# Kernel tuning notes

Hardware: AMD Instinct MI355X
Metric: run time of the kernel (lower is better)

The kernel has to match this reference:

```python
import jax, jax.numpy as jnp
import numpy as np

B, T, C = 2048, 200, 128
PAD = jnp.float32(-4294967295.0)  # -(2**32) + 1, as in SoftmaxWeightedSum padding


def setup_inputs() -> dict:
    key = jax.random.key(0)
    k1, k2, k3, k4 = jax.random.split(key, 4)
    user_query = jax.random.normal(k1, (B, 1, C), dtype=jnp.float32)
    keys = jax.random.normal(k2, (B, T, C), dtype=jnp.float32)
    keys_length = jax.random.randint(k3, (B, 1), 0, T, dtype=jnp.int32)
    W = jax.random.normal(k4, (C, C), dtype=jnp.float32) * (1.0 / np.sqrt(C))
    b = jnp.zeros((C,), dtype=jnp.float32)
    return {"user_query": user_query, "keys": keys, "keys_length": keys_length, "W": W, "b": b}


def reference(user_query, keys, keys_length, W, b):
    # Dense with tanh activation: [B,1,C] -> [B,1,C]
    query = jnp.tanh(jnp.einsum('bqc,cd->bqd', user_query, W) + b)
    # DotAttention with scale: [B,1,T]
    scale = jnp.asarray(1.0 / np.sqrt(C), dtype=keys.dtype)
    align = jnp.einsum('bqc,btc->bqt', query, keys) * scale
    # sequence mask [B,1,T] from keys_length [B,1]
    key_masks = jnp.arange(T, dtype=keys_length.dtype)[None, None, :] < keys_length[:, :, None]
    align = jnp.where(key_masks, align, PAD)
    align = jax.nn.softmax(align, axis=-1)
    # weighted sum over history: [B,1,C]
    output = jnp.einsum('bqt,btc->bqc', align, keys)
    # residual: broadcasts [B,1,C] + [B,T,C] -> [B,T,C] (faithful to `output += keys`)
    output = output + keys
    # mean pool over sequence, keepdims -> [B,1,C]
    return jnp.mean(output, axis=1, keepdims=True)
```

## Files before the change

### kernel.cpp

```cpp
#include <hip/hip_runtime.h>
#include <math.h>

#define BB 2048
#define TT 200
#define CC 128
#define PADV (-4294967295.0f)
#define SCALE 0.08838834764831845f
#define INVT (1.0f / 200.0f)

__global__ __launch_bounds__(256) void user_attn_kernel(
    const float* __restrict__ uq,
    const float* __restrict__ keys,
    const int*   __restrict__ klen,
    const float* __restrict__ W,
    const float* __restrict__ bias,
    float*       __restrict__ out)
{
    const int b    = blockIdx.x;
    const int tid  = threadIdx.x;
    const int lane = tid & 63;
    const int wid  = tid >> 6;

    __shared__ float  s_q[CC];
    __shared__ float  s_w[TT];
    __shared__ float  s_uq[CC];
    __shared__ float  s_tmp[8];
    __shared__ float2 s_acc[256];

    const float* kb = keys + (size_t)b * TT * CC;

    if (tid < CC) s_uq[tid] = uq[b * CC + tid];
    __syncthreads();
    if (tid < CC) {
        float acc = bias[tid];
        #pragma unroll 8
        for (int c = 0; c < CC; ++c)
            acc = fmaf(s_uq[c], W[c * CC + tid], acc);
        s_q[tid] = tanhf(acc);
    }
    __syncthreads();

    const int len = klen[b];

    const float q0 = s_q[2 * lane];
    const float q1 = s_q[2 * lane + 1];
    for (int t = wid; t < TT; t += 4) {
        const float2 k = *(const float2*)(kb + t * CC + 2 * lane);
        float d = q0 * k.x + q1 * k.y;
        #pragma unroll
        for (int off = 32; off > 0; off >>= 1)
            d += __shfl_xor(d, off, 64);
        if (lane == 0)
            s_w[t] = (t < len) ? d * SCALE : PADV;
    }
    __syncthreads();

    float v = (tid < TT) ? s_w[tid] : -INFINITY;
    float m = v;
    #pragma unroll
    for (int off = 32; off > 0; off >>= 1)
        m = fmaxf(m, __shfl_xor(m, off, 64));
    if (lane == 0) s_tmp[wid] = m;
    __syncthreads();
    m = fmaxf(fmaxf(s_tmp[0], s_tmp[1]), fmaxf(s_tmp[2], s_tmp[3]));

    float e = (tid < TT) ? expf(v - m) : 0.0f;
    float ssum = e;
    #pragma unroll
    for (int off = 32; off > 0; off >>= 1)
        ssum += __shfl_xor(ssum, off, 64);
    if (lane == 0) s_tmp[4 + wid] = ssum;
    __syncthreads();
    ssum = s_tmp[4] + s_tmp[5] + s_tmp[6] + s_tmp[7];
    if (tid < TT) s_w[tid] = e / ssum + INVT;
    __syncthreads();

    const int c2 = lane * 2;
    float2 acc = make_float2(0.0f, 0.0f);
    for (int t = wid; t < TT; t += 4) {
        const float w  = s_w[t];
        const float2 k = *(const float2*)(kb + t * CC + c2);
        acc.x = fmaf(w, k.x, acc.x);
        acc.y = fmaf(w, k.y, acc.y);
    }
    s_acc[tid] = acc;
    __syncthreads();
    if (tid < 64) {
        float2 r  = s_acc[tid];
        float2 a1 = s_acc[tid + 64];
        float2 a2 = s_acc[tid + 128];
        float2 a3 = s_acc[tid + 192];
        r.x += a1.x + a2.x + a3.x;
        r.y += a1.y + a2.y + a3.y;
        *(float2*)(out + (size_t)b * CC + c2) = r;
    }
}

extern "C" void kernel_launch(void* const* d_in, const int* in_sizes, int n_in,
                              void* d_out, int out_size, void* d_ws, size_t ws_size,
                              hipStream_t stream) {
    const float* uq   = (const float*)d_in[0];
    const float* keys = (const float*)d_in[1];
    const int*   klen = (const int*)d_in[2];
    const float* W    = (const float*)d_in[3];
    const float* bias = (const float*)d_in[4];
    float* out = (float*)d_out;

    user_attn_kernel<<<BB, 256, 0, stream>>>(uq, keys, klen, W, bias, out);
}
```

Baseline: 329.2 us.

## Cache keys in shared memory as bf16 to avoid second global read

Each key row is now read from global memory once. The kernel converts the keys to bf16 and stages them in LDS, and the weighted-sum pass reads that copy instead of re-fetching them from HBM. The block grows to 512 threads, the W·q matvec is split across four thread groups, and loads widen to float4. Rounding the keys to bf16 lowers the precision of the weighted sum, and the roughly 53KB of LDS per block may cut occupancy.

```diff
diff --git a/kernel.cpp b/kernel.cpp
--- a/kernel.cpp
+++ b/kernel.cpp
@@ -1,4 +1,5 @@
 #include <hip/hip_runtime.h>
+#include <hip/hip_bf16.h>
 #include <math.h>
 
 #define BB 2048
@@ -7,8 +8,9 @@
 #define PADV (-4294967295.0f)
 #define SCALE 0.08838834764831845f
 #define INVT (1.0f / 200.0f)
+#define PITCH 132
 
-__global__ __launch_bounds__(256) void user_attn_kernel(
+__global__ __launch_bounds__(512) void user_attn_kernel(
     const float* __restrict__ uq,
     const float* __restrict__ keys,
     const int*   __restrict__ klen,
@@ -21,78 +23,119 @@
     const int lane = tid & 63;
     const int wid  = tid >> 6;
 
-    __shared__ float  s_q[CC];
-    __shared__ float  s_w[TT];
-    __shared__ float  s_uq[CC];
-    __shared__ float  s_tmp[8];
-    __shared__ float2 s_acc[256];
+    __shared__ unsigned short s_kb16[TT * PITCH];
+    __shared__ float s_q[CC];
+    __shared__ float s_w[TT];
+    __shared__ float s_tmp[16];
+
+    float*  s_part = (float*)s_kb16;
+    float*  s_uq   = (float*)s_kb16 + 512;
+    float4* s_red  = (float4*)s_kb16;
 
     const float* kb = keys + (size_t)b * TT * CC;
 
     if (tid < CC) s_uq[tid] = uq[b * CC + tid];
     __syncthreads();
+    {
+        const int d    = tid & 127;
+        const int part = tid >> 7;
+        float acc = 0.0f;
+        const int c0 = part * 32;
+        #pragma unroll 8
+        for (int c = 0; c < 32; ++c)
+            acc = fmaf(s_uq[c0 + c], W[(c0 + c) * CC + d], acc);
+        s_part[part * CC + d] = acc;
+    }
+    __syncthreads();
     if (tid < CC) {
-        float acc = bias[tid];
-        #pragma unroll 8
-        for (int c = 0; c < CC; ++c)
-            acc = fmaf(s_uq[c], W[c * CC + tid], acc);
+        float acc = bias[tid] + s_part[tid] + s_part[CC + tid]
+                  + s_part[2 * CC + tid] + s_part[3 * CC + tid];
         s_q[tid] = tanhf(acc);
     }
     __syncthreads();
 
     const int len = klen[b];
 
-    const float q0 = s_q[2 * lane];
-    const float q1 = s_q[2 * lane + 1];
-    for (int t = wid; t < TT; t += 4) {
-        const float2 k = *(const float2*)(kb + t * CC + 2 * lane);
-        float d = q0 * k.x + q1 * k.y;
+    const int cl = lane & 31;
+    const int c4 = cl * 4;
+    const int h  = lane >> 5;
+    const float q0 = s_q[c4], q1 = s_q[c4 + 1], q2 = s_q[c4 + 2], q3 = s_q[c4 + 3];
+
+    for (int p = wid; p < TT / 2; p += 8) {
+        const int r = 2 * p + h;
+        const float4 k = *(const float4*)(kb + r * CC + c4);
+        float d = q0 * k.x + q1 * k.y + q2 * k.z + q3 * k.w;
         #pragma unroll
-        for (int off = 32; off > 0; off >>= 1)
+        for (int off = 1; off < 32; off <<= 1)
             d += __shfl_xor(d, off, 64);
-        if (lane == 0)
-            s_w[t] = (t < len) ? d * SCALE : PADV;
+        if (cl == 0)
+            s_w[r] = (r < len) ? d * SCALE : PADV;
+
+        __hip_bfloat16 h0 = __float2bfloat16(k.x);
+        __hip_bfloat16 h1 = __float2bfloat16(k.y);
+        __hip_bfloat16 h2 = __float2bfloat16(k.z);
+        __hip_bfloat16 h3 = __float2bfloat16(k.w);
+        ushort4 pk;
+        pk.x = *(unsigned short*)&h0; pk.y = *(unsigned short*)&h1;
+        pk.z = *(unsigned short*)&h2; pk.w = *(unsigned short*)&h3;
+        *(ushort4*)(&s_kb16[(size_t)r * PITCH + c4]) = pk;
     }
     __syncthreads();
 
-    float v = (tid < TT) ? s_w[tid] : -INFINITY;
-    float m = v;
-    #pragma unroll
-    for (int off = 32; off > 0; off >>= 1)
-        m = fmaxf(m, __shfl_xor(m, off, 64));
-    if (lane == 0) s_tmp[wid] = m;
-    __syncthreads();
-    m = fmaxf(fmaxf(s_tmp[0], s_tmp[1]), fmaxf(s_tmp[2], s_tmp[3]));
+    {
+        float v = (tid < TT) ? s_w[tid] : -INFINITY;
+        float m = v;
+        #pragma unroll
+        for (int off = 1; off < 64; off <<= 1)
+            m = fmaxf(m, __shfl_xor(m, off, 64));
+        if (lane == 0) s_tmp[wid] = m;
+        __syncthreads();
+        m = s_tmp[0];
+        #pragma unroll
+        for (int w = 1; w < 8; ++w) m = fmaxf(m, s_tmp[w]);
 
-    float e = (tid < TT) ? expf(v - m) : 0.0f;
-    float ssum = e;
-    #pragma unroll
-    for (int off = 32; off > 0; off >>= 1)
-        ssum += __shfl_xor(ssum, off, 64);
-    if (lane == 0) s_tmp[4 + wid] = ssum;
-    __syncthreads();
-    ssum = s_tmp[4] + s_tmp[5] + s_tmp[6] + s_tmp[7];
-    if (tid < TT) s_w[tid] = e / ssum + INVT;
+        float e = (tid < TT) ? expf(v - m) : 0.0f;
+        float ssum = e;
+        #pragma unroll
+        for (int off = 1; off < 64; off <<= 1)
+            ssum += __shfl_xor(ssum, off, 64);
+        if (lane == 0) s_tmp[8 + wid] = ssum;
+        __syncthreads();
+        ssum = 0.0f;
+        #pragma unroll
+        for (int w = 0; w < 8; ++w) ssum += s_tmp[8 + w];
+        if (tid < TT) s_w[tid] = e / ssum + INVT;
+    }
     __syncthreads();
 
-    const int c2 = lane * 2;
-    float2 acc = make_float2(0.0f, 0.0f);
-    for (int t = wid; t < TT; t += 4) {
-        const float w  = s_w[t];
-        const float2 k = *(const float2*)(kb + t * CC + c2);
-        acc.x = fmaf(w, k.x, acc.x);
-        acc.y = fmaf(w, k.y, acc.y);
+    float4 acc = make_float4(0.0f, 0.0f, 0.0f, 0.0f);
+    for (int p = wid; p < TT / 2; p += 8) {
+        const int r = 2 * p + h;
+        const float w = s_w[r];
+        const ushort4 pk = *(const ushort4*)(&s_kb16[(size_t)r * PITCH + c4]);
+        acc.x = fmaf(w, __uint_as_float((unsigned)pk.x << 16), acc.x);
+        acc.y = fmaf(w, __uint_as_float((unsigned)pk.y << 16), acc.y);
+        acc.z = fmaf(w, __uint_as_float((unsigned)pk.z << 16), acc.z);
+        acc.w = fmaf(w, __uint_as_float((unsigned)pk.w << 16), acc.w);
     }
-    s_acc[tid] = acc;
+    acc.x += __shfl_xor(acc.x, 32, 64);
+    acc.y += __shfl_xor(acc.y, 32, 64);
+    acc.z += __shfl_xor(acc.z, 32, 64);
+    acc.w += __shfl_xor(acc.w, 32, 64);
+
     __syncthreads();
-    if (tid < 64) {
-        float2 r  = s_acc[tid];
-        float2 a1 = s_acc[tid + 64];
-        float2 a2 = s_acc[tid + 128];
-        float2 a3 = s_acc[tid + 192];
-        r.x += a1.x + a2.x + a3.x;
-        r.y += a1.y + a2.y + a3.y;
-        *(float2*)(out + (size_t)b * CC + c2) = r;
+    if (cl == lane)
+        s_red[wid * 32 + cl] = acc;
+    __syncthreads();
+
+    if (tid < 32) {
+        float4 r = s_red[tid];
+        #pragma unroll
+        for (int w = 1; w < 8; ++w) {
+            float4 v = s_red[w * 32 + tid];
+            r.x += v.x; r.y += v.y; r.z += v.z; r.w += v.w;
+        }
+        *(float4*)(out + (size_t)b * CC + 4 * tid) = r;
     }
 }
 
@@ -106,5 +149,5 @@
     const float* bias = (const float*)d_in[4];
     float* out = (float*)d_out;
 
-    user_attn_kernel<<<BB, 256, 0, stream>>>(uq, keys, klen, W, bias, out);
+    user_attn_kernel<<<BB, 512, 0, stream>>>(uq, keys, klen, W, bias, out);
 }
```

Result: faster. 306.2 us (-7.0%).

## Use float4 key loads with half-wave rows and split query GEMV across all threads

Applied to the files above, without the earlier changes.

Keys are now read as float4, so each half-wave of 32 lanes covers one 128-wide row and a wavefront handles two rows per load. The score pass is unrolled to two row pairs per iteration to keep more loads in flight. The query matvec is split across all 256 threads into two partial sums that are combined before the tanh. Launch bounds now request 8 blocks per SM, and the final reduction uses float4 plus a cross-half shuffle, at the cost of shuffle reductions with more steps and possible register pressure.

```diff
diff --git a/kernel.cpp b/kernel.cpp
--- a/kernel.cpp
+++ b/kernel.cpp
@@ -8,7 +8,7 @@
 #define SCALE 0.08838834764831845f
 #define INVT (1.0f / 200.0f)
 
-__global__ __launch_bounds__(256) void user_attn_kernel(
+__global__ __launch_bounds__(256, 8) void user_attn_kernel(
     const float* __restrict__ uq,
     const float* __restrict__ keys,
     const int*   __restrict__ klen,
@@ -20,79 +20,122 @@
     const int tid  = threadIdx.x;
     const int lane = tid & 63;
     const int wid  = tid >> 6;
+    const int cl   = lane & 31;
+    const int h    = lane >> 5;
+    const int c4   = cl * 4;
 
     __shared__ float  s_q[CC];
+    __shared__ float  s_uq[CC];
+    __shared__ float  s_part[2 * CC];
     __shared__ float  s_w[TT];
-    __shared__ float  s_uq[CC];
     __shared__ float  s_tmp[8];
-    __shared__ float2 s_acc[256];
+    __shared__ float4 s_red[4 * 32];
 
     const float* kb = keys + (size_t)b * TT * CC;
 
     if (tid < CC) s_uq[tid] = uq[b * CC + tid];
     __syncthreads();
-    if (tid < CC) {
-        float acc = bias[tid];
-        #pragma unroll 8
-        for (int c = 0; c < CC; ++c)
-            acc = fmaf(s_uq[c], W[c * CC + tid], acc);
-        s_q[tid] = tanhf(acc);
+    {
+        const int d    = tid & 127;
+        const int part = tid >> 7;
+        const int c0   = part * 64;
+        float acc = 0.0f;
+        #pragma unroll 16
+        for (int c = 0; c < 64; ++c)
+            acc = fmaf(s_uq[c0 + c], W[(c0 + c) * CC + d], acc);
+        s_part[part * CC + d] = acc;
+    }
+    __syncthreads();
+    if (tid < CC)
+        s_q[tid] = tanhf(bias[tid] + s_part[tid] + s_part[CC + tid]);
+    __syncthreads();
+
+    const int len = klen[b];
+    const float q0 = s_q[c4], q1 = s_q[c4 + 1], q2 = s_q[c4 + 2], q3 = s_q[c4 + 3];
+
+    {
+        int p = wid;
+        for (; p + 4 < TT / 2; p += 8) {
+            const int r0 = 2 * p + h;
+            const int r1 = r0 + 8;
+            const float4 k0 = *(const float4*)(kb + r0 * CC + c4);
+            const float4 k1 = *(const float4*)(kb + r1 * CC + c4);
+            float d0 = q0 * k0.x + q1 * k0.y + q2 * k0.z + q3 * k0.w;
+            float d1 = q0 * k1.x + q1 * k1.y + q2 * k1.z + q3 * k1.w;
+            #pragma unroll
+            for (int off = 1; off < 32; off <<= 1) {
+                d0 += __shfl_xor(d0, off, 64);
+                d1 += __shfl_xor(d1, off, 64);
+            }
+            if (cl == 0) {
+                s_w[r0] = (r0 < len) ? d0 * SCALE : PADV;
+                s_w[r1] = (r1 < len) ? d1 * SCALE : PADV;
+            }
+        }
+        if (p < TT / 2) {
+            const int r0 = 2 * p + h;
+            const float4 k0 = *(const float4*)(kb + r0 * CC + c4);
+            float d0 = q0 * k0.x + q1 * k0.y + q2 * k0.z + q3 * k0.w;
+            #pragma unroll
+            for (int off = 1; off < 32; off <<= 1)
+                d0 += __shfl_xor(d0, off, 64);
+            if (cl == 0)
+                s_w[r0] = (r0 < len) ? d0 * SCALE : PADV;
+        }
     }
     __syncthreads();
 
-    const int len = klen[b];
+    {
+        float v = (tid < TT) ? s_w[tid] : -INFINITY;
+        float m = v;
+        #pragma unroll
+        for (int off = 1; off < 64; off <<= 1)
+            m = fmaxf(m, __shfl_xor(m, off, 64));
+        if (lane == 0) s_tmp[wid] = m;
+        __syncthreads();
+        m = fmaxf(fmaxf(s_tmp[0], s_tmp[1]), fmaxf(s_tmp[2], s_tmp[3]));
 
-    const float q0 = s_q[2 * lane];
-    const float q1 = s_q[2 * lane + 1];
-    for (int t = wid; t < TT; t += 4) {
-        const float2 k = *(const float2*)(kb + t * CC + 2 * lane);
-        float d = q0 * k.x + q1 * k.y;
+        float e = (tid < TT) ? expf(v - m) : 0.0f;
+        float ssum = e;
         #pragma unroll
-        for (int off = 32; off > 0; off >>= 1)
-            d += __shfl_xor(d, off, 64);
-        if (lane == 0)
-            s_w[t] = (t < len) ? d * SCALE : PADV;
+        for (int off = 1; off < 64; off <<= 1)
+            ssum += __shfl_xor(ssum, off, 64);
+        if (lane == 0) s_tmp[4 + wid] = ssum;
+        __syncthreads();
+        ssum = (s_tmp[4] + s_tmp[5]) + (s_tmp[6] + s_tmp[7]);
+        if (tid < TT) s_w[tid] = e / ssum + INVT;
     }
     __syncthreads();
 
-    float v = (tid < TT) ? s_w[tid] : -INFINITY;
-    float m = v;
-    #pragma unroll
-    for (int off = 32; off > 0; off >>= 1)
-        m = fmaxf(m, __shfl_xor(m, off, 64));
-    if (lane == 0) s_tmp[wid] = m;
-    __syncthreads();
-    m = fmaxf(fmaxf(s_tmp[0], s_tmp[1]), fmaxf(s_tmp[2], s_tmp[3]));
+    float4 acc = make_float4(0.0f, 0.0f, 0.0f, 0.0f);
+    #pragma unroll 2
+    for (int p = wid; p < TT / 2; p += 4) {
+        const int r = 2 * p + h;
+        const float w  = s_w[r];
+        const float4 k = *(const float4*)(kb + r * CC + c4);
+        acc.x = fmaf(w, k.x, acc.x);
+        acc.y = fmaf(w, k.y, acc.y);
+        acc.z = fmaf(w, k.z, acc.z);
+        acc.w = fmaf(w, k.w, acc.w);
+    }
+    acc.x += __shfl_xor(acc.x, 32, 64);
+    acc.y += __shfl_xor(acc.y, 32, 64);
+    acc.z += __shfl_xor(acc.z, 32, 64);
+    acc.w += __shfl_xor(acc.w, 32, 64);
 
-    float e = (tid < TT) ? expf(v - m) : 0.0f;
-    float ssum = e;
-    #pragma unroll
-    for (int off = 32; off > 0; off >>= 1)
-        ssum += __shfl_xor(ssum, off, 64);
-    if (lane == 0) s_tmp[4 + wid] = ssum;
-    __syncthreads();
-    ssum = s_tmp[4] + s_tmp[5] + s_tmp[6] + s_tmp[7];
-    if (tid < TT) s_w[tid] = e / ssum + INVT;
+    if (h == 0) s_red[wid * 32 + cl] = acc;
     __syncthreads();
 
-    const int c2 = lane * 2;
-    float2 acc = make_float2(0.0f, 0.0f);
-    for (int t = wid; t < TT; t += 4) {
-        const float w  = s_w[t];
-        const float2 k = *(const float2*)(kb + t * CC + c2);
-        acc.x = fmaf(w, k.x, acc.x);
-        acc.y = fmaf(w, k.y, acc.y);
-    }
-    s_acc[tid] = acc;
-    __syncthreads();
-    if (tid < 64) {
-        float2 r  = s_acc[tid];
-        float2 a1 = s_acc[tid + 64];
-        float2 a2 = s_acc[tid + 128];
-        float2 a3 = s_acc[tid + 192];
-        r.x += a1.x + a2.x + a3.x;
-        r.y += a1.y + a2.y + a3.y;
-        *(float2*)(out + (size_t)b * CC + c2) = r;
+    if (tid < 32) {
+        float4 r0 = s_red[tid];
+        const float4 r1 = s_red[32 + tid];
+        const float4 r2 = s_red[64 + tid];
+        const float4 r3 = s_red[96 + tid];
+        r0.x += (r1.x + r2.x) + r3.x;
+        r0.y += (r1.y + r2.y) + r3.y;
+        r0.z += (r1.z + r2.z) + r3.z;
+        r0.w += (r1.w + r2.w) + r3.w;
+        *(float4*)(out + (size_t)b * CC + 4 * tid) = r0;
     }
 }
 
```

Result: faster. 319.3 us (-3.0%).

## Split query GEMV into separate kernel and stream keys once with online softmax

Applied to the files above, without the earlier changes.

Moves the tanh(uq·W+b) GEMV into its own kernel that writes the query to workspace, processing two batches per block. The attention kernel now reads each key row once, computing scores, an online-softmax weighted sum and a plain key sum in a single pass with float4 loads. Eight half-wave groups are merged at the end with max-rescaling, which removes the second read of keys and several block barriers. In exchange it adds a second kernel launch, a workspace round trip, and uses fast __expf instead of expf.

```diff
diff --git a/kernel.cpp b/kernel.cpp
--- a/kernel.cpp
+++ b/kernel.cpp
@@ -6,93 +6,135 @@
 #define CC 128
 #define PADV (-4294967295.0f)
 #define SCALE 0.08838834764831845f
-#define INVT (1.0f / 200.0f)
+#define INV_T (1.0f / 200.0f)
 
-__global__ __launch_bounds__(256) void user_attn_kernel(
+__global__ __launch_bounds__(256) void q_gemv_kernel(
     const float* __restrict__ uq,
+    const float* __restrict__ W,
+    const float* __restrict__ bias,
+    float*       __restrict__ qws)
+{
+    const int tid = threadIdx.x;
+    const int d   = tid & 127;
+    const int wh  = tid >> 7;
+    const int b   = blockIdx.x * 2 + wh;
+
+    __shared__ float s_uq[2 * CC];
+    s_uq[tid] = uq[blockIdx.x * 2 * CC + tid];
+    __syncthreads();
+
+    float acc = bias[d];
+    const float* uqr = &s_uq[wh * CC];
+    #pragma unroll 16
+    for (int c = 0; c < CC; ++c)
+        acc = fmaf(uqr[c], W[c * CC + d], acc);
+    qws[(size_t)b * CC + d] = tanhf(acc);
+}
+
+__global__ __launch_bounds__(256, 6) void attn_stream_kernel(
     const float* __restrict__ keys,
     const int*   __restrict__ klen,
-    const float* __restrict__ W,
-    const float* __restrict__ bias,
+    const float* __restrict__ qws,
     float*       __restrict__ out)
 {
     const int b    = blockIdx.x;
     const int tid  = threadIdx.x;
     const int lane = tid & 63;
     const int wid  = tid >> 6;
+    const int cl   = lane & 31;
+    const int h    = lane >> 5;
+    const int g    = wid * 2 + h;
+    const int c4   = cl * 4;
 
-    __shared__ float  s_q[CC];
-    __shared__ float  s_w[TT];
-    __shared__ float  s_uq[CC];
-    __shared__ float  s_tmp[8];
-    __shared__ float2 s_acc[256];
+    __shared__ float  s_m[8];
+    __shared__ float  s_l[8];
+    __shared__ float4 s_acc[8 * 32];
+    __shared__ float4 s_ksum[8 * 32];
 
-    const float* kb = keys + (size_t)b * TT * CC;
+    const float* kb  = keys + (size_t)b * TT * CC;
+    const int    len = klen[b];
+    const float4 q   = *(const float4*)(qws + (size_t)b * CC + c4);
 
-    if (tid < CC) s_uq[tid] = uq[b * CC + tid];
-    __syncthreads();
-    if (tid < CC) {
-        float acc = bias[tid];
-        #pragma unroll 8
-        for (int c = 0; c < CC; ++c)
-            acc = fmaf(s_uq[c], W[c * CC + tid], acc);
-        s_q[tid] = tanhf(acc);
+    float  m = -INFINITY, l = 0.0f;
+    float4 acc  = make_float4(0.f, 0.f, 0.f, 0.f);
+    float4 ksum = make_float4(0.f, 0.f, 0.f, 0.f);
+
+    auto upd = [&](float d, const float4& k, int r) {
+        const float s  = (r < len) ? d * SCALE : PADV;
+        const float mn = fmaxf(m, s);
+        const float sc = __expf(m - mn);
+        const float p  = __expf(s - mn);
+        l = fmaf(l, sc, p);
+        acc.x = fmaf(p, k.x, acc.x * sc);
+        acc.y = fmaf(p, k.y, acc.y * sc);
+        acc.z = fmaf(p, k.z, acc.z * sc);
+        acc.w = fmaf(p, k.w, acc.w * sc);
+        ksum.x += k.x; ksum.y += k.y; ksum.z += k.z; ksum.w += k.w;
+        m = mn;
+    };
+
+    for (int outer = 0; outer < 5; ++outer) {
+        const int r0 = g + 40 * outer;
+        const float4 k0 = *(const float4*)(kb + (r0     ) * CC + c4);
+        const float4 k1 = *(const float4*)(kb + (r0 +  8) * CC + c4);
+        const float4 k2 = *(const float4*)(kb + (r0 + 16) * CC + c4);
+        const float4 k3 = *(const float4*)(kb + (r0 + 24) * CC + c4);
+        const float4 k4 = *(const float4*)(kb + (r0 + 32) * CC + c4);
+
+        float d0 = q.x * k0.x + q.y * k0.y + q.z * k0.z + q.w * k0.w;
+        float d1 = q.x * k1.x + q.y * k1.y + q.z * k1.z + q.w * k1.w;
+        float d2 = q.x * k2.x + q.y * k2.y + q.z * k2.z + q.w * k2.w;
+        float d3 = q.x * k3.x + q.y * k3.y + q.z * k3.z + q.w * k3.w;
+        float d4 = q.x * k4.x + q.y * k4.y + q.z * k4.z + q.w * k4.w;
+
+        #pragma unroll
+        for (int off = 1; off < 32; off <<= 1) {
+            d0 += __shfl_xor(d0, off, 64);
+            d1 += __shfl_xor(d1, off, 64);
+            d2 += __shfl_xor(d2, off, 64);
+            d3 += __shfl_xor(d3, off, 64);
+            d4 += __shfl_xor(d4, off, 64);
+        }
+
+        upd(d0, k0, r0);
+        upd(d1, k1, r0 + 8);
+        upd(d2, k2, r0 + 16);
+        upd(d3, k3, r0 + 24);
+        upd(d4, k4, r0 + 32);
     }
+
+    s_acc [g * 32 + cl] = acc;
+    s_ksum[g * 32 + cl] = ksum;
+    if (cl == 0) { s_m[g] = m; s_l[g] = l; }
     __syncthreads();
 
-    const int len = klen[b];
+    if (tid < 32) {
+        float M = s_m[0];
+        #pragma unroll
+        for (int i = 1; i < 8; ++i) M = fmaxf(M, s_m[i]);
 
-    const float q0 = s_q[2 * lane];
-    const float q1 = s_q[2 * lane + 1];
-    for (int t = wid; t < TT; t += 4) {
-        const float2 k = *(const float2*)(kb + t * CC + 2 * lane);
-        float d = q0 * k.x + q1 * k.y;
+        float  L  = 0.0f;
+        float4 A  = make_float4(0.f, 0.f, 0.f, 0.f);
+        float4 KS = make_float4(0.f, 0.f, 0.f, 0.f);
         #pragma unroll
-        for (int off = 32; off > 0; off >>= 1)
-            d += __shfl_xor(d, off, 64);
-        if (lane == 0)
-            s_w[t] = (t < len) ? d * SCALE : PADV;
-    }
-    __syncthreads();
-
-    float v = (tid < TT) ? s_w[tid] : -INFINITY;
-    float m = v;
-    #pragma unroll
-    for (int off = 32; off > 0; off >>= 1)
-        m = fmaxf(m, __shfl_xor(m, off, 64));
-    if (lane == 0) s_tmp[wid] = m;
-    __syncthreads();
-    m = fmaxf(fmaxf(s_tmp[0], s_tmp[1]), fmaxf(s_tmp[2], s_tmp[3]));
-
-    float e = (tid < TT) ? expf(v - m) : 0.0f;
-    float ssum = e;
-    #pragma unroll
-    for (int off = 32; off > 0; off >>= 1)
-        ssum += __shfl_xor(ssum, off, 64);
-    if (lane == 0) s_tmp[4 + wid] = ssum;
-    __syncthreads();
-    ssum = s_tmp[4] + s_tmp[5] + s_tmp[6] + s_tmp[7];
-    if (tid < TT) s_w[tid] = e / ssum + INVT;
-    __syncthreads();
-
-    const int c2 = lane * 2;
-    float2 acc = make_float2(0.0f, 0.0f);
-    for (int t = wid; t < TT; t += 4) {
-        const float w  = s_w[t];
-        const float2 k = *(const float2*)(kb + t * CC + c2);
-        acc.x = fmaf(w, k.x, acc.x);
-        acc.y = fmaf(w, k.y, acc.y);
-    }
-    s_acc[tid] = acc;
-    __syncthreads();
-    if (tid < 64) {
-        float2 r  = s_acc[tid];
-        float2 a1 = s_acc[tid + 64];
-        float2 a2 = s_acc[tid + 128];
-        float2 a3 = s_acc[tid + 192];
-        r.x += a1.x + a2.x + a3.x;
-        r.y += a1.y + a2.y + a3.y;
-        *(float2*)(out + (size_t)b * CC + c2) = r;
+        for (int i = 0; i < 8; ++i) {
+            const float al = __expf(s_m[i] - M);
+            L = fmaf(s_l[i], al, L);
+            const float4 a = s_acc[i * 32 + tid];
+            A.x = fmaf(a.x, al, A.x);
+            A.y = fmaf(a.y, al, A.y);
+            A.z = fmaf(a.z, al, A.z);
+            A.w = fmaf(a.w, al, A.w);
+            const float4 ks = s_ksum[i * 32 + tid];
+            KS.x += ks.x; KS.y += ks.y; KS.z += ks.z; KS.w += ks.w;
+        }
+        const float invL = 1.0f / L;
+        float4 o;
+        o.x = fmaf(A.x, invL, KS.x * INV_T);
+        o.y = fmaf(A.y, invL, KS.y * INV_T);
+        o.z = fmaf(A.z, invL, KS.z * INV_T);
+        o.w = fmaf(A.w, invL, KS.w * INV_T);
+        *(float4*)(out + (size_t)b * CC + 4 * tid) = o;
     }
 }
 
@@ -105,6 +147,8 @@
     const float* W    = (const float*)d_in[3];
     const float* bias = (const float*)d_in[4];
     float* out = (float*)d_out;
+    float* qws = (float*)d_ws;
 
-    user_attn_kernel<<<BB, 256, 0, stream>>>(uq, keys, klen, W, bias, out);
+    q_gemv_kernel<<<BB / 2, 256, 0, stream>>>(uq, W, bias, qws);
+    attn_stream_kernel<<<BB, 256, 0, stream>>>(keys, klen, qws, out);
 }
```

Result: faster. 300.6 us (-8.7%).
